# Kernel optimization log

Hardware: AMD Instinct MI355X
Metric: run time of the kernel (lower is better)

## Reference

```python
import jax, jax.numpy as jnp
import numpy as np

T, B, I, H = 512, 64, 256, 512  # seq_len, batch, input_size, hidden_size


def setup_inputs() -> dict:
    key = jax.random.key(0)
    ks = jax.random.split(key, 16)
    s_i = 1.0 / np.sqrt(I)
    s_h = 1.0 / np.sqrt(H)
    d = {
        "x": jax.random.normal(ks[0], (T, B, I), dtype=jnp.float32),
        # layer 0 (input I -> H)
        "w_ih0": jax.random.normal(ks[1], (4 * H, I), dtype=jnp.float32) * s_i,
        "w_hh0": jax.random.normal(ks[2], (4 * H, H), dtype=jnp.float32) * s_h,
        "b_ih0": jax.random.normal(ks[3], (4 * H,), dtype=jnp.float32),
        "b_hh0": jax.random.normal(ks[4], (4 * H,), dtype=jnp.float32),
        "p_i0": jax.random.normal(ks[5], (H,), dtype=jnp.float32),
        "p_f0": jax.random.normal(ks[6], (H,), dtype=jnp.float32),
        "p_o0": jax.random.normal(ks[7], (H,), dtype=jnp.float32),
        # layer 1 (H -> H)
        "w_ih1": jax.random.normal(ks[8], (4 * H, H), dtype=jnp.float32) * s_h,
        "w_hh1": jax.random.normal(ks[9], (4 * H, H), dtype=jnp.float32) * s_h,
        "b_ih1": jax.random.normal(ks[10], (4 * H,), dtype=jnp.float32),
        "b_hh1": jax.random.normal(ks[11], (4 * H,), dtype=jnp.float32),
        "p_i1": jax.random.normal(ks[12], (H,), dtype=jnp.float32),
        "p_f1": jax.random.normal(ks[13], (H,), dtype=jnp.float32),
        "p_o1": jax.random.normal(ks[14], (H,), dtype=jnp.float32),
    }
    return d


def _cell(inp, h, c, w_ih, w_hh, b_ih, b_hh, p_i, p_f, p_o):
    # gates: [B, 4H]
    gates = inp @ w_ih.T + h @ w_hh.T + (b_ih + b_hh)
    ig, fg, gg, og = jnp.split(gates, 4, axis=1)
    ig = jax.nn.sigmoid(ig + c * p_i)
    fg = jax.nn.sigmoid(fg + c * p_f)
    gg = jnp.tanh(gg)
    og = jax.nn.sigmoid(og + c * p_o)
    c_new = fg * c + ig * gg
    h_new = og * jnp.tanh(c_new)
    return h_new, c_new


def reference(x, w_ih0, w_hh0, b_ih0, b_hh0, p_i0, p_f0, p_o0,
              w_ih1, w_hh1, b_ih1, b_hh1, p_i1, p_f1, p_o1):
    sg = jax.lax.stop_gradient  # replicates .detach() in the torch code
    B_, H_ = x.shape[1], w_hh0.shape[1]
    z = jnp.zeros((B_, H_), dtype=x.dtype)

    def step(carry, xt):
        h0, c0, h1, c1 = carry
        h0n, c0n = _cell(xt, sg(h0), sg(c0), w_ih0, w_hh0, b_ih0, b_hh0, p_i0, p_f0, p_o0)
        # layer 1 input is the PREVIOUS timestep's layer-0 hidden (detached),
        # exactly as in the torch code where h is reassigned after the cell loop
        h1n, c1n = _cell(sg(h0), sg(h1), sg(c1), w_ih1, w_hh1, b_ih1, b_hh1, p_i1, p_f1, p_o1)
        return (h0n, c0n, h1n, c1n), h1n

    (h0, c0, h1, c1), outputs = jax.lax.scan(step, (z, z, z, z), x)
    h_n = jnp.stack([h0, h1], axis=0)  # [num_layers, B, H]
    c_n = jnp.stack([c0, c1], axis=0)
    return outputs, h_n, c_n
```

## Files before the change

kernel.cpp:

```cpp
#include <hip/hip_runtime.h>

#define TT 512
#define BB 64
#define II 256
#define HH 512
#define BH (BB * HH)

#define OF_H0B0 0
#define OF_H1B0 (BH)
#define OF_CT0  (2 * BH)
#define OF_CT1  (3 * BH)
#define OF_H0B1 (4 * BH)
#define OF_H1B1 (5 * BH)

__device__ __forceinline__ float sigf(float v) {
    return 1.0f / (1.0f + __expf(-v));
}

__global__ __launch_bounds__(256, 1) void lstm_step(
    const float* __restrict__ x,
    const float* __restrict__ wih0, const float* __restrict__ whh0,
    const float* __restrict__ bih0, const float* __restrict__ bhh0,
    const float* __restrict__ pi0,  const float* __restrict__ pf0,
    const float* __restrict__ po0,
    const float* __restrict__ wih1, const float* __restrict__ whh1,
    const float* __restrict__ bih1, const float* __restrict__ bhh1,
    const float* __restrict__ pi1,  const float* __restrict__ pf1,
    const float* __restrict__ po1,
    float* __restrict__ ws, float* __restrict__ out, int t)
{
    __shared__ float4 lds4[2][64 * 32];

    const int tid = threadIdx.x;
    const int b   = tid & 63;
    const int jju = __builtin_amdgcn_readfirstlane(tid >> 6);
    const int blk = blockIdx.x;
    const int L   = blk >> 7;
    const int jb  = blk & 127;
    const int j   = jb * 4 + jju;

    const int rp = t & 1;
    const float* __restrict__ h0r = ws + (rp ? OF_H0B1 : OF_H0B0);
    const float* __restrict__ h1r = ws + (rp ? OF_H1B1 : OF_H1B0);
    float* __restrict__ h0w = ws + (rp ? OF_H0B0 : OF_H0B1);
    float* __restrict__ h1w = ws + (rp ? OF_H1B0 : OF_H1B1);
    float* __restrict__ cT  = ws + (L ? OF_CT1 : OF_CT0);

    const int NC     = L ? 8 : 6;
    const int firstB = L ? 4 : 2;

    const float* __restrict__ WA = L ? wih1 : wih0;
    const float* __restrict__ WB = L ? whh1 : whh0;
    const int rlA = L ? HH : II;

    const int sb  = tid >> 2;
    const int skf = tid & 3;

    float4 sreg0, sreg1, sreg2, sreg3, sreg4, sreg5, sreg6, sreg7;

    const float* srow_for = nullptr;

#define STAGE_LOAD(c)                                                        \
    {                                                                        \
        const float* srow;                                                   \
        if (L == 0) {                                                        \
            if ((c) < 2) srow = x + ((size_t)t * BB + sb) * II + (c) * 128;  \
            else         srow = h0r + (size_t)sb * HH + ((c) - 2) * 128;     \
        } else {                                                             \
            if ((c) < 4) srow = h0r + (size_t)sb * HH + (c) * 128;           \
            else         srow = h1r + (size_t)sb * HH + ((c) - 4) * 128;     \
        }                                                                    \
        sreg0 = *(const float4*)(srow + (skf + 4 * 0) * 4);                  \
        sreg1 = *(const float4*)(srow + (skf + 4 * 1) * 4);                  \
        sreg2 = *(const float4*)(srow + (skf + 4 * 2) * 4);                  \
        sreg3 = *(const float4*)(srow + (skf + 4 * 3) * 4);                  \
        sreg4 = *(const float4*)(srow + (skf + 4 * 4) * 4);                  \
        sreg5 = *(const float4*)(srow + (skf + 4 * 5) * 4);                  \
        sreg6 = *(const float4*)(srow + (skf + 4 * 6) * 4);                  \
        sreg7 = *(const float4*)(srow + (skf + 4 * 7) * 4);                  \
    }

#define STAGE_WRITE(buf)                                                     \
    {                                                                        \
        const int sw = sb & 7;                                               \
        float4* Lw = &lds4[(buf)][sb * 32];                                  \
        Lw[(skf + 4 * 0) ^ sw] = sreg0;                                      \
        Lw[(skf + 4 * 1) ^ sw] = sreg1;                                      \
        Lw[(skf + 4 * 2) ^ sw] = sreg2;                                      \
        Lw[(skf + 4 * 3) ^ sw] = sreg3;                                      \
        Lw[(skf + 4 * 4) ^ sw] = sreg4;                                      \
        Lw[(skf + 4 * 5) ^ sw] = sreg5;                                      \
        Lw[(skf + 4 * 6) ^ sw] = sreg6;                                      \
        Lw[(skf + 4 * 7) ^ sw] = sreg7;                                      \
    }

    (void)srow_for;

    float4 A0 = {0, 0, 0, 0}, A1 = {0, 0, 0, 0};
    float4 A2 = {0, 0, 0, 0}, A3 = {0, 0, 0, 0};

    STAGE_LOAD(0);
    STAGE_WRITE(0);

    const int swz   = b & 7;
    const float4* __restrict__ LbBase0 = &lds4[0][b * 32];
    const float4* __restrict__ LbBase1 = &lds4[1][b * 32];

    for (int c = 0; c < NC; ++c) {
        const float4 *Wp0, *Wp1, *Wp2, *Wp3;
        if (c < firstB) {
            const int koff = c * 128;
            Wp0 = (const float4*)(WA + (size_t)(0 * HH + j) * rlA + koff);
            Wp1 = (const float4*)(WA + (size_t)(1 * HH + j) * rlA + koff);
            Wp2 = (const float4*)(WA + (size_t)(2 * HH + j) * rlA + koff);
            Wp3 = (const float4*)(WA + (size_t)(3 * HH + j) * rlA + koff);
        } else {
            const int koff = (c - firstB) * 128;
            Wp0 = (const float4*)(WB + (size_t)(0 * HH + j) * HH + koff);
            Wp1 = (const float4*)(WB + (size_t)(1 * HH + j) * HH + koff);
            Wp2 = (const float4*)(WB + (size_t)(2 * HH + j) * HH + koff);
            Wp3 = (const float4*)(WB + (size_t)(3 * HH + j) * HH + koff);
        }

        if (c + 1 < NC) STAGE_LOAD(c + 1);

        __syncthreads();

        const float4* __restrict__ Lb = (c & 1) ? LbBase1 : LbBase0;
#pragma unroll 4
        for (int kk = 0; kk < 32; ++kk) {
            const float4 h4 = Lb[kk ^ swz];
            const float4 w0 = Wp0[kk], w1 = Wp1[kk], w2 = Wp2[kk], w3 = Wp3[kk];
            A0.x += h4.x * w0.x; A0.y += h4.y * w0.y; A0.z += h4.z * w0.z; A0.w += h4.w * w0.w;
            A1.x += h4.x * w1.x; A1.y += h4.y * w1.y; A1.z += h4.z * w1.z; A1.w += h4.w * w1.w;
            A2.x += h4.x * w2.x; A2.y += h4.y * w2.y; A2.z += h4.z * w2.z; A2.w += h4.w * w2.w;
            A3.x += h4.x * w3.x; A3.y += h4.y * w3.y; A3.z += h4.z * w3.z; A3.w += h4.w * w3.w;
        }

        if (c + 1 < NC) STAGE_WRITE((c + 1) & 1);
    }

    const float* __restrict__ bih = L ? bih1 : bih0;
    const float* __restrict__ bhh = L ? bhh1 : bhh0;
    const float* __restrict__ pi  = L ? pi1 : pi0;
    const float* __restrict__ pf  = L ? pf1 : pf0;
    const float* __restrict__ po  = L ? po1 : po0;

    const float a0 = A0.x + A0.y + A0.z + A0.w + bih[0 * HH + j] + bhh[0 * HH + j];
    const float a1 = A1.x + A1.y + A1.z + A1.w + bih[1 * HH + j] + bhh[1 * HH + j];
    const float a2 = A2.x + A2.y + A2.z + A2.w + bih[2 * HH + j] + bhh[2 * HH + j];
    const float a3 = A3.x + A3.y + A3.z + A3.w + bih[3 * HH + j] + bhh[3 * HH + j];

    const float c_old = cT[j * 64 + b];
    const float ig = sigf(a0 + c_old * pi[j]);
    const float fg = sigf(a1 + c_old * pf[j]);
    const float gg = tanhf(a2);
    const float og = sigf(a3 + c_old * po[j]);
    const float cn = fg * c_old + ig * gg;
    const float hn = og * tanhf(cn);

    cT[j * 64 + b] = cn;
    if (L == 0) {
        h0w[(size_t)b * HH + j] = hn;
    } else {
        h1w[(size_t)b * HH + j] = hn;
        out[(size_t)t * BH + (size_t)b * HH + j] = hn;
    }
#undef STAGE_LOAD
#undef STAGE_WRITE
}

__global__ __launch_bounds__(256, 1) void cn_fixup(const float* __restrict__ ws,
                                                   float* __restrict__ out)
{
    const int idx = blockIdx.x * 256 + threadIdx.x;
    const int l = idx >> 15;
    const int r = idx & 32767;
    const int jrow = r >> 6;
    const int b = r & 63;
    const float v = ws[(l ? OF_CT1 : OF_CT0) + jrow * 64 + b];
    out[(size_t)TT * BH + 2 * BH + (size_t)l * BH + (size_t)b * HH + jrow] = v;
}

extern "C" void kernel_launch(void* const* d_in, const int* in_sizes, int n_in,
                              void* d_out, int out_size, void* d_ws, size_t ws_size,
                              hipStream_t stream) {
    (void)in_sizes; (void)n_in; (void)out_size; (void)ws_size;

    const float* x    = (const float*)d_in[0];
    const float* wih0 = (const float*)d_in[1];
    const float* whh0 = (const float*)d_in[2];
    const float* bih0 = (const float*)d_in[3];
    const float* bhh0 = (const float*)d_in[4];
    const float* pi0  = (const float*)d_in[5];
    const float* pf0  = (const float*)d_in[6];
    const float* po0  = (const float*)d_in[7];
    const float* wih1 = (const float*)d_in[8];
    const float* whh1 = (const float*)d_in[9];
    const float* bih1 = (const float*)d_in[10];
    const float* bhh1 = (const float*)d_in[11];
    const float* pi1  = (const float*)d_in[12];
    const float* pf1  = (const float*)d_in[13];
    const float* po1  = (const float*)d_in[14];

    float* ws  = (float*)d_ws;
    float* out = (float*)d_out;

    hipMemsetAsync(ws, 0, (size_t)(4 * BH) * sizeof(float), stream);

    for (int t = 0; t < TT; ++t) {
        lstm_step<<<256, 256, 0, stream>>>(
            x, wih0, whh0, bih0, bhh0, pi0, pf0, po0,
            wih1, whh1, bih1, bhh1, pi1, pf1, po1,
            ws, out, t);
    }

    hipMemcpyAsync(out + (size_t)TT * BH, ws, (size_t)(2 * BH) * sizeof(float),
                   hipMemcpyDeviceToDevice, stream);
    cn_fixup<<<256, 256, 0, stream>>>(ws, out);
}
```

Measured before the change: 18.33 ms.

## Split K across four waves per output with LDS reduction, 1024-thread blocks

Each block now uses 1024 threads: every output column's dot product is split four ways along K across waves, with partial sums reduced through a shared-memory combine buffer before the gate math. The staging of inputs is reorganized into fewer, larger phases (256 or 128 wide) with a 32-way XOR swizzle. The aim is to raise per-CU wave count and shorten each wave's serial K loop, which hides weight-load latency in this latency-bound per-timestep kernel. In exchange it adds an extra barrier and LDS reduction, leaves three quarters of the threads idle during the epilogue, and uses more LDS per block.

After: 17.84 ms. 2.7% less time.

```diff
diff --git a/kernel.cpp b/kernel.cpp
--- a/kernel.cpp
+++ b/kernel.cpp
@@ -17,7 +17,9 @@
     return 1.0f / (1.0f + __expf(-v));
 }
 
-__global__ __launch_bounds__(256, 1) void lstm_step(
+#define SWZ(g, r) ((((g) & ~31)) | ((((g) & 31)) ^ ((r) & 31)))
+
+__global__ __launch_bounds__(1024, 4) void lstm_step(
     const float* __restrict__ x,
     const float* __restrict__ wih0, const float* __restrict__ whh0,
     const float* __restrict__ bih0, const float* __restrict__ bhh0,
@@ -29,15 +31,17 @@
     const float* __restrict__ po1,
     float* __restrict__ ws, float* __restrict__ out, int t)
 {
-    __shared__ float4 lds4[2][64 * 32];
+    __shared__ float4 buf[2][64 * 64];
+    __shared__ float  comb[4][4][4][64];
 
     const int tid = threadIdx.x;
     const int b   = tid & 63;
-    const int jju = __builtin_amdgcn_readfirstlane(tid >> 6);
+    const int wv  = tid >> 6;
+    const int jj  = __builtin_amdgcn_readfirstlane(wv >> 2);
+    const int ksq = __builtin_amdgcn_readfirstlane(wv & 3);
     const int blk = blockIdx.x;
     const int L   = blk >> 7;
-    const int jb  = blk & 127;
-    const int j   = jb * 4 + jju;
+    const int j   = (blk & 127) * 4 + jj;
 
     const int rp = t & 1;
     const float* __restrict__ h0r = ws + (rp ? OF_H0B1 : OF_H0B0);
@@ -46,128 +50,137 @@
     float* __restrict__ h1w = ws + (rp ? OF_H1B0 : OF_H1B1);
     float* __restrict__ cT  = ws + (L ? OF_CT1 : OF_CT0);
 
-    const int NC     = L ? 8 : 6;
-    const int firstB = L ? 4 : 2;
-
-    const float* __restrict__ WA = L ? wih1 : wih0;
-    const float* __restrict__ WB = L ? whh1 : whh0;
-    const int rlA = L ? HH : II;
-
-    const int sb  = tid >> 2;
-    const int skf = tid & 3;
-
-    float4 sreg0, sreg1, sreg2, sreg3, sreg4, sreg5, sreg6, sreg7;
-
-    const float* srow_for = nullptr;
-
-#define STAGE_LOAD(c)                                                        \
-    {                                                                        \
-        const float* srow;                                                   \
-        if (L == 0) {                                                        \
-            if ((c) < 2) srow = x + ((size_t)t * BB + sb) * II + (c) * 128;  \
-            else         srow = h0r + (size_t)sb * HH + ((c) - 2) * 128;     \
-        } else {                                                             \
-            if ((c) < 4) srow = h0r + (size_t)sb * HH + (c) * 128;           \
-            else         srow = h1r + (size_t)sb * HH + ((c) - 4) * 128;     \
-        }                                                                    \
-        sreg0 = *(const float4*)(srow + (skf + 4 * 0) * 4);                  \
-        sreg1 = *(const float4*)(srow + (skf + 4 * 1) * 4);                  \
-        sreg2 = *(const float4*)(srow + (skf + 4 * 2) * 4);                  \
-        sreg3 = *(const float4*)(srow + (skf + 4 * 3) * 4);                  \
-        sreg4 = *(const float4*)(srow + (skf + 4 * 4) * 4);                  \
-        sreg5 = *(const float4*)(srow + (skf + 4 * 5) * 4);                  \
-        sreg6 = *(const float4*)(srow + (skf + 4 * 6) * 4);                  \
-        sreg7 = *(const float4*)(srow + (skf + 4 * 7) * 4);                  \
-    }
-
-#define STAGE_WRITE(buf)                                                     \
-    {                                                                        \
-        const int sw = sb & 7;                                               \
-        float4* Lw = &lds4[(buf)][sb * 32];                                  \
-        Lw[(skf + 4 * 0) ^ sw] = sreg0;                                      \
-        Lw[(skf + 4 * 1) ^ sw] = sreg1;                                      \
-        Lw[(skf + 4 * 2) ^ sw] = sreg2;                                      \
-        Lw[(skf + 4 * 3) ^ sw] = sreg3;                                      \
-        Lw[(skf + 4 * 4) ^ sw] = sreg4;                                      \
-        Lw[(skf + 4 * 5) ^ sw] = sreg5;                                      \
-        Lw[(skf + 4 * 6) ^ sw] = sreg6;                                      \
-        Lw[(skf + 4 * 7) ^ sw] = sreg7;                                      \
-    }
-
-    (void)srow_for;
+    const int NP = L ? 4 : 5;
+#define PH_NK(p) (L ? 256 : ((p) == 0 ? 256 : 128))
+#define PH_SRC(p)                                                          \
+    (L == 0 ? ((p) == 0 ? x + ((size_t)t * BB + sr) * II                   \
+                        : h0r + (size_t)sr * HH + ((p) - 1) * 128)         \
+            : ((p) < 2 ? h0r + (size_t)sr * HH + (p) * 256                 \
+                       : h1r + (size_t)sr * HH + ((p) - 2) * 256))
+
+    const int sr = tid >> 4;
+    const int sf = tid & 15;
+
+    float4 sreg0, sreg1, sreg2, sreg3;
+    sreg2 = make_float4(0.f, 0.f, 0.f, 0.f);
+    sreg3 = sreg2;
+
+#define STAGE_LOAD(p)                                                      \
+    {                                                                      \
+        const int nk_ = PH_NK(p);                                          \
+        const float* __restrict__ src_ = PH_SRC(p);                        \
+        sreg0 = *(const float4*)(src_ + 4 * sf);                           \
+        sreg1 = *(const float4*)(src_ + 4 * (sf + 16));                    \
+        if (nk_ == 256) {                                                  \
+            sreg2 = *(const float4*)(src_ + 4 * (sf + 32));                \
+            sreg3 = *(const float4*)(src_ + 4 * (sf + 48));                \
+        }                                                                  \
+    }
+
+#define STAGE_WRITE(p, bb)                                                 \
+    {                                                                      \
+        const int nk_ = PH_NK(p);                                          \
+        const int rs_ = nk_ >> 2;                                          \
+        float4* __restrict__ B_ = &buf[bb][(size_t)sr * rs_];              \
+        B_[SWZ(sf, sr)]      = sreg0;                                      \
+        B_[SWZ(sf + 16, sr)] = sreg1;                                      \
+        if (nk_ == 256) {                                                  \
+            B_[SWZ(sf + 32, sr)] = sreg2;                                  \
+            B_[SWZ(sf + 48, sr)] = sreg3;                                  \
+        }                                                                  \
+    }
 
     float4 A0 = {0, 0, 0, 0}, A1 = {0, 0, 0, 0};
     float4 A2 = {0, 0, 0, 0}, A3 = {0, 0, 0, 0};
 
+#define COMPUTE(p, bb)                                                         \
+    {                                                                          \
+        const int nk_  = PH_NK(p);                                             \
+        const int GRW_ = nk_ >> 4;             \
+        const int rs_  = nk_ >> 2;                 \
+        const float* W_; int rowlen_, koff_;                                   \
+        if (L == 0) {                                                          \
+            if ((p) == 0) { W_ = wih0; rowlen_ = II; koff_ = ksq * 64; }       \
+            else { W_ = whh0; rowlen_ = HH; koff_ = ((p) - 1) * 128 + ksq * 32; } \
+        } else {                                                               \
+            if ((p) < 2) { W_ = wih1; rowlen_ = HH; koff_ = (p) * 256 + ksq * 64; } \
+            else { W_ = whh1; rowlen_ = HH; koff_ = ((p) - 2) * 256 + ksq * 64; } \
+        }                                                                      \
+        const float4* __restrict__ Wp0_ =                                      \
+            (const float4*)(W_ + (size_t)(0 * HH + j) * rowlen_ + koff_);      \
+        const float4* __restrict__ Wp1_ =                                      \
+            (const float4*)(W_ + (size_t)(1 * HH + j) * rowlen_ + koff_);      \
+        const float4* __restrict__ Wp2_ =                                      \
+            (const float4*)(W_ + (size_t)(2 * HH + j) * rowlen_ + koff_);      \
+        const float4* __restrict__ Wp3_ =                                      \
+            (const float4*)(W_ + (size_t)(3 * HH + j) * rowlen_ + koff_);      \
+        const float4* __restrict__ Bb_ = &buf[bb][(size_t)b * rs_];            \
+        const int g0_ = ksq * GRW_;                                            \
+        _Pragma("unroll 2")                                                    \
+        for (int i_ = 0; i_ < GRW_; ++i_) {                                    \
+            const int g_ = g0_ + i_;                                           \
+            const float4 h4 = Bb_[SWZ(g_, b)];                                 \
+            const float4 w0 = Wp0_[i_], w1 = Wp1_[i_], w2 = Wp2_[i_], w3 = Wp3_[i_]; \
+            A0.x += h4.x * w0.x; A0.y += h4.y * w0.y; A0.z += h4.z * w0.z; A0.w += h4.w * w0.w; \
+            A1.x += h4.x * w1.x; A1.y += h4.y * w1.y; A1.z += h4.z * w1.z; A1.w += h4.w * w1.w; \
+            A2.x += h4.x * w2.x; A2.y += h4.y * w2.y; A2.z += h4.z * w2.z; A2.w += h4.w * w2.w; \
+            A3.x += h4.x * w3.x; A3.y += h4.y * w3.y; A3.z += h4.z * w3.z; A3.w += h4.w * w3.w; \
+        }                                                                      \
+    }
+
     STAGE_LOAD(0);
-    STAGE_WRITE(0);
-
-    const int swz   = b & 7;
-    const float4* __restrict__ LbBase0 = &lds4[0][b * 32];
-    const float4* __restrict__ LbBase1 = &lds4[1][b * 32];
-
-    for (int c = 0; c < NC; ++c) {
-        const float4 *Wp0, *Wp1, *Wp2, *Wp3;
-        if (c < firstB) {
-            const int koff = c * 128;
-            Wp0 = (const float4*)(WA + (size_t)(0 * HH + j) * rlA + koff);
-            Wp1 = (const float4*)(WA + (size_t)(1 * HH + j) * rlA + koff);
-            Wp2 = (const float4*)(WA + (size_t)(2 * HH + j) * rlA + koff);
-            Wp3 = (const float4*)(WA + (size_t)(3 * HH + j) * rlA + koff);
+    STAGE_WRITE(0, 0);
+
+    for (int p = 0; p < NP; ++p) {
+        __syncthreads();
+        if (p + 1 < NP) STAGE_LOAD(p + 1);
+        COMPUTE(p, p & 1);
+        if (p + 1 < NP) STAGE_WRITE(p + 1, (p + 1) & 1);
+    }
+
+    comb[jj][ksq][0][b] = A0.x + A0.y + A0.z + A0.w;
+    comb[jj][ksq][1][b] = A1.x + A1.y + A1.z + A1.w;
+    comb[jj][ksq][2][b] = A2.x + A2.y + A2.z + A2.w;
+    comb[jj][ksq][3][b] = A3.x + A3.y + A3.z + A3.w;
+    __syncthreads();
+
+    if (ksq == 0) {
+        const float* __restrict__ bih = L ? bih1 : bih0;
+        const float* __restrict__ bhh = L ? bhh1 : bhh0;
+        const float* __restrict__ pi  = L ? pi1 : pi0;
+        const float* __restrict__ pf  = L ? pf1 : pf0;
+        const float* __restrict__ po  = L ? po1 : po0;
+
+        const float a0 = comb[jj][0][0][b] + comb[jj][1][0][b] + comb[jj][2][0][b] + comb[jj][3][0][b]
+                       + bih[0 * HH + j] + bhh[0 * HH + j];
+        const float a1 = comb[jj][0][1][b] + comb[jj][1][1][b] + comb[jj][2][1][b] + comb[jj][3][1][b]
+                       + bih[1 * HH + j] + bhh[1 * HH + j];
+        const float a2 = comb[jj][0][2][b] + comb[jj][1][2][b] + comb[jj][2][2][b] + comb[jj][3][2][b]
+                       + bih[2 * HH + j] + bhh[2 * HH + j];
+        const float a3 = comb[jj][0][3][b] + comb[jj][1][3][b] + comb[jj][2][3][b] + comb[jj][3][3][b]
+                       + bih[3 * HH + j] + bhh[3 * HH + j];
+
+        const float c_old = cT[j * 64 + b];
+        const float ig = sigf(a0 + c_old * pi[j]);
+        const float fg = sigf(a1 + c_old * pf[j]);
+        const float gg = tanhf(a2);
+        const float og = sigf(a3 + c_old * po[j]);
+        const float cn = fg * c_old + ig * gg;
+        const float hn = og * tanhf(cn);
+
+        cT[j * 64 + b] = cn;
+        if (L == 0) {
+            h0w[(size_t)b * HH + j] = hn;
         } else {
-            const int koff = (c - firstB) * 128;
-            Wp0 = (const float4*)(WB + (size_t)(0 * HH + j) * HH + koff);
-            Wp1 = (const float4*)(WB + (size_t)(1 * HH + j) * HH + koff);
-            Wp2 = (const float4*)(WB + (size_t)(2 * HH + j) * HH + koff);
-            Wp3 = (const float4*)(WB + (size_t)(3 * HH + j) * HH + koff);
+            h1w[(size_t)b * HH + j] = hn;
+            out[(size_t)t * BH + (size_t)b * HH + j] = hn;
         }
-
-        if (c + 1 < NC) STAGE_LOAD(c + 1);
-
-        __syncthreads();
-
-        const float4* __restrict__ Lb = (c & 1) ? LbBase1 : LbBase0;
-#pragma unroll 4
-        for (int kk = 0; kk < 32; ++kk) {
-            const float4 h4 = Lb[kk ^ swz];
-            const float4 w0 = Wp0[kk], w1 = Wp1[kk], w2 = Wp2[kk], w3 = Wp3[kk];
-            A0.x += h4.x * w0.x; A0.y += h4.y * w0.y; A0.z += h4.z * w0.z; A0.w += h4.w * w0.w;
-            A1.x += h4.x * w1.x; A1.y += h4.y * w1.y; A1.z += h4.z * w1.z; A1.w += h4.w * w1.w;
-            A2.x += h4.x * w2.x; A2.y += h4.y * w2.y; A2.z += h4.z * w2.z; A2.w += h4.w * w2.w;
-            A3.x += h4.x * w3.x; A3.y += h4.y * w3.y; A3.z += h4.z * w3.z; A3.w += h4.w * w3.w;
-        }
-
-        if (c + 1 < NC) STAGE_WRITE((c + 1) & 1);
-    }
-
-    const float* __restrict__ bih = L ? bih1 : bih0;
-    const float* __restrict__ bhh = L ? bhh1 : bhh0;
-    const float* __restrict__ pi  = L ? pi1 : pi0;
-    const float* __restrict__ pf  = L ? pf1 : pf0;
-    const float* __restrict__ po  = L ? po1 : po0;
-
-    const float a0 = A0.x + A0.y + A0.z + A0.w + bih[0 * HH + j] + bhh[0 * HH + j];
-    const float a1 = A1.x + A1.y + A1.z + A1.w + bih[1 * HH + j] + bhh[1 * HH + j];
-    const float a2 = A2.x + A2.y + A2.z + A2.w + bih[2 * HH + j] + bhh[2 * HH + j];
-    const float a3 = A3.x + A3.y + A3.z + A3.w + bih[3 * HH + j] + bhh[3 * HH + j];
-
-    const float c_old = cT[j * 64 + b];
-    const float ig = sigf(a0 + c_old * pi[j]);
-    const float fg = sigf(a1 + c_old * pf[j]);
-    const float gg = tanhf(a2);
-    const float og = sigf(a3 + c_old * po[j]);
-    const float cn = fg * c_old + ig * gg;
-    const float hn = og * tanhf(cn);
-
-    cT[j * 64 + b] = cn;
-    if (L == 0) {
-        h0w[(size_t)b * HH + j] = hn;
-    } else {
-        h1w[(size_t)b * HH + j] = hn;
-        out[(size_t)t * BH + (size_t)b * HH + j] = hn;
-    }
+    }
+#undef PH_NK
+#undef PH_SRC
 #undef STAGE_LOAD
 #undef STAGE_WRITE
+#undef COMPUTE
 }
 
 __global__ __launch_bounds__(256, 1) void cn_fixup(const float* __restrict__ ws,
@@ -209,7 +222,7 @@
     hipMemsetAsync(ws, 0, (size_t)(4 * BH) * sizeof(float), stream);
 
     for (int t = 0; t < TT; ++t) {
-        lstm_step<<<256, 256, 0, stream>>>(
+        lstm_step<<<256, 1024, 0, stream>>>(
             x, wih0, whh0, bih0, bhh0, pi0, pf0, po0,
             wih1, whh1, bih1, bhh1, pi1, pf1, po1,
             ws, out, t);
```
